# Performance work log

Measured on AMD Instinct MI355X. Metric: run time of the kernel, lower is better.

Reference implementation:

```python
import jax, jax.numpy as jnp
import numpy as np

RES = 7          # pooler_resolution
SR = 2           # sampling_ratio
SCALES = (0.25, 0.125, 0.0625)  # 1/stride for the 3 FPN levels


def _bilinear(feat, ys, xs):
    # feat [C,H,W]; ys, xs [N,S,S] sample coords; returns [C,N,S,S]
    C, H, W = feat.shape
    valid = (ys > -1.0) & (ys < H) & (xs > -1.0) & (xs < W)
    y = jnp.clip(ys, 0.0, H - 1)
    x = jnp.clip(xs, 0.0, W - 1)
    y0 = jnp.floor(y).astype(jnp.int32)
    x0 = jnp.floor(x).astype(jnp.int32)
    y1 = jnp.minimum(y0 + 1, H - 1)
    x1 = jnp.minimum(x0 + 1, W - 1)
    ly = y - y0; lx = x - x0
    hy = 1.0 - ly; hx = 1.0 - lx
    v = (feat[:, y0, x0] * (hy * hx) + feat[:, y0, x1] * (hy * lx)
         + feat[:, y1, x0] * (ly * hx) + feat[:, y1, x1] * (ly * lx))
    return v * valid


def _roi_align(feat, boxes, scale):
    # feat [C,H,W], boxes [N,4] (t,l,b,r) in image coords, aligned=True
    t, l, b, r = (boxes[:, 0], boxes[:, 1], boxes[:, 2], boxes[:, 3])
    sy = t * scale - 0.5
    sx = l * scale - 0.5
    bh = (b - t) * scale / RES
    bw = (r - l) * scale / RES
    S = RES * SR
    g = (jnp.arange(S, dtype=feat.dtype) + 0.5) / SR  # sample offsets in bin units
    ys = sy[:, None] + g[None, :] * bh[:, None]  # [N,S]
    xs = sx[:, None] + g[None, :] * bw[:, None]
    N = boxes.shape[0]
    Y = jnp.broadcast_to(ys[:, :, None], (N, S, S))
    X = jnp.broadcast_to(xs[:, None, :], (N, S, S))
    v = _bilinear(feat, Y, X)                      # [C,N,S,S]
    C = feat.shape[0]
    v = v.reshape(C, N, RES, SR, RES, SR).mean(axis=(3, 5))
    return jnp.transpose(v, (1, 0, 2, 3))          # [N,C,RES,RES]


def _forward(feat0, feat1, feat2, bbox2d, anchor_id,
             fc1_w, fc1_b, bn1_g, bn1_b, fc2_w, fc2_b, bn2_g, bn2_b,
             cate_w, cate_b, bbox3d_w, bbox3d_b, yawc_w, yawc_b,
             yawr_w, yawr_b, hgt_w, hgt_b):
    # yxhw -> tlbr (mu.convert_box_format_yxhw_to_tlbr)
    cy, cx, h, w = (bbox2d[..., 0], bbox2d[..., 1], bbox2d[..., 2], bbox2d[..., 3])
    tlbr = jnp.stack([cy - h / 2, cx - w / 2, cy + h / 2, cx + w / 2], axis=-1)
    level = anchor_id // 3  # [B,N] per-box FPN level (anchor_id // 3 == i routing)
    feats = [feat0, feat1, feat2]
    B, N = level.shape
    C = feat0.shape[1]
    pooled = jnp.zeros((B, N, C, RES, RES), dtype=feat0.dtype)
    for i in range(3):
        al = jax.vmap(lambda fm, bx, s=SCALES[i]: _roi_align(fm, bx, s))(feats[i], tlbr)
        pooled = jnp.where((level == i)[:, :, None, None, None], al, pooled)
    x = pooled.reshape(B * N, -1)  # [B*N, C*RES*RES]
    eps = 1e-5
    for Wt, bb, g2, b2 in ((fc1_w, fc1_b, bn1_g, bn1_b), (fc2_w, fc2_b, bn2_g, bn2_b)):
        x = x @ Wt + bb
        mu = x.mean(0)
        var = x.var(0)
        x = jax.nn.relu((x - mu) / jnp.sqrt(var + eps) * g2 + b2)
    cate = x @ cate_w + cate_b
    bbox3d = x @ bbox3d_w + bbox3d_b
    yawc = x @ yawc_w + yawc_b
    yawr = x @ yawr_w + yawr_b
    hgt = x @ hgt_w + hgt_b
    out = jnp.concatenate([cate, bbox3d, yawc, yawr, hgt], axis=-1)  # [B*N, 100]
    return out.reshape(B, N, -1)


def setup_inputs() -> dict:
    key = jax.random.key(0)
    ks = jax.random.split(key, 24)
    B, N, C = 4, 512, 256
    FC = 1024
    IMG = 512.0
    NUM_CLASSES, BOX_DIM, BINS = 3, 6, 12
    feat0 = jax.random.normal(ks[0], (B, C, 128, 128), jnp.float32)
    feat1 = jax.random.normal(ks[1], (B, C, 64, 64), jnp.float32)
    feat2 = jax.random.normal(ks[2], (B, C, 32, 32), jnp.float32)
    cy = jax.random.uniform(ks[3], (B, N)) * IMG
    cx = jax.random.uniform(ks[4], (B, N)) * IMG
    h = 16.0 + jax.random.uniform(ks[5], (B, N)) * 240.0
    w = 16.0 + jax.random.uniform(ks[6], (B, N)) * 240.0
    bbox2d = jnp.stack([cy, cx, h, w], axis=-1)
    anchor_id = jax.random.randint(ks[7], (B, N), 0, 9, dtype=jnp.int32)
    in_dim = C * RES * RES  # 12544
    fc1_w = jax.random.normal(ks[8], (in_dim, FC), jnp.float32) / np.sqrt(in_dim)
    fc1_b = jnp.zeros((FC,), jnp.float32)
    bn1_g = jnp.ones((FC,), jnp.float32)
    bn1_b = jnp.zeros((FC,), jnp.float32)
    fc2_w = jax.random.normal(ks[9], (FC, FC), jnp.float32) / np.sqrt(FC)
    fc2_b = jnp.zeros((FC,), jnp.float32)
    bn2_g = jnp.ones((FC,), jnp.float32)
    bn2_b = jnp.zeros((FC,), jnp.float32)
    cate_w = jax.random.normal(ks[10], (FC, NUM_CLASSES + 1), jnp.float32) * 0.01
    cate_b = jnp.zeros((NUM_CLASSES + 1,), jnp.float32)
    bbox3d_w = jax.random.normal(ks[11], (FC, NUM_CLASSES * BOX_DIM), jnp.float32) * 0.001
    bbox3d_b = jnp.zeros((NUM_CLASSES * BOX_DIM,), jnp.float32)
    yawc_w = jax.random.normal(ks[12], (FC, NUM_CLASSES * BINS), jnp.float32) * 0.001
    yawc_b = jnp.zeros((NUM_CLASSES * BINS,), jnp.float32)
    yawr_w = jax.random.normal(ks[13], (FC, NUM_CLASSES * BINS), jnp.float32) * 0.001
    yawr_b = jnp.zeros((NUM_CLASSES * BINS,), jnp.float32)
    hgt_w = jax.random.normal(ks[14], (FC, NUM_CLASSES * 2), jnp.float32) * 0.001
    hgt_b = jnp.zeros((NUM_CLASSES * 2,), jnp.float32)
    return {
        'feat0': feat0, 'feat1': feat1, 'feat2': feat2,
        'bbox2d': bbox2d, 'anchor_id': anchor_id,
        'fc1_w': fc1_w, 'fc1_b': fc1_b, 'bn1_g': bn1_g, 'bn1_b': bn1_b,
        'fc2_w': fc2_w, 'fc2_b': fc2_b, 'bn2_g': bn2_g, 'bn2_b': bn2_b,
        'cate_w': cate_w, 'cate_b': cate_b, 'bbox3d_w': bbox3d_w, 'bbox3d_b': bbox3d_b,
        'yawc_w': yawc_w, 'yawc_b': yawc_b, 'yawr_w': yawr_w, 'yawr_b': yawr_b,
        'hgt_w': hgt_w, 'hgt_b': hgt_b,
    }


def reference(feat0, feat1, feat2, bbox2d, anchor_id,
              fc1_w, fc1_b, bn1_g, bn1_b, fc2_w, fc2_b, bn2_g, bn2_b,
              cate_w, cate_b, bbox3d_w, bbox3d_b, yawc_w, yawc_b,
              yawr_w, yawr_b, hgt_w, hgt_b):
    return _forward(feat0, feat1, feat2, bbox2d, anchor_id,
                    fc1_w, fc1_b, bn1_g, bn1_b, fc2_w, fc2_b, bn2_g, bn2_b,
                    cate_w, cate_b, bbox3d_w, bbox3d_b, yawc_w, yawc_b,
                    yawr_w, yawr_b, hgt_w, hgt_b)
```

## Files before the change

kernel.cpp:

```cpp
#include <hip/hip_runtime.h>
#include <hip/hip_bf16.h>

typedef unsigned short u16;
typedef unsigned int u32;
typedef __bf16 bf16x8 __attribute__((ext_vector_type(8)));
typedef float f32x4 __attribute__((ext_vector_type(4)));

#define RESOLUTION 7
#define SR 2
#define SS 14
#define NSAMP 196

static __device__ __forceinline__ u16 f2bf(float f) {
    __hip_bfloat16 t = __float2bfloat16(f);
    return *reinterpret_cast<u16*>(&t);
}
static __device__ __forceinline__ float bf2f(u16 h) {
    return __uint_as_float(((u32)h) << 16);
}

static __device__ __forceinline__ void load_lds16(const u16* g, u16* l) {
    __builtin_amdgcn_global_load_lds(
        (const __attribute__((address_space(1))) unsigned int*)g,
        (__attribute__((address_space(3))) unsigned int*)l, 16, 0, 0);
}

__global__ __launch_bounds__(256) void transpose_feat_kernel(
    const float* __restrict__ in, u16* __restrict__ out, int HW) {
    int b = blockIdx.y;
    int hw0 = blockIdx.x * 64;
    __shared__ u16 tile[256][65];

    int hwo = threadIdx.x & 63;
    int c0 = threadIdx.x >> 6;
    for (int cc = 0; cc < 256; cc += 4) {
        int c = cc + c0;
        float v = in[((size_t)(b * 256 + c)) * HW + hw0 + hwo];
        tile[c][hwo] = f2bf(v);
    }
    __syncthreads();

    int ro = threadIdx.x >> 5;
    int co = (threadIdx.x & 31) * 8;
    for (int i = 0; i < 64; i += 8) {
        int hw = i + ro;
        union { uint4 v; u16 h[8]; } o;
        #pragma unroll
        for (int j = 0; j < 8; ++j) o.h[j] = tile[co + j][hw];
        *(uint4*)&out[((size_t)b * HW + hw0 + hw) * 256 + co] = o.v;
    }
}

__global__ __launch_bounds__(256) void transpose_w_kernel(
    const float* __restrict__ in, u16* __restrict__ out, int K, int perm) {
    int kp0 = blockIdx.x * 64, n0 = blockIdx.y * 64;
    __shared__ u16 tile[64][65];

    int nn = threadIdx.x & 63, ks = threadIdx.x >> 6;
    for (int i = 0; i < 64; i += 4) {
        int kp = kp0 + ks + i;
        int k = perm ? ((kp & 255) * 49 + (kp >> 8)) : kp;
        tile[ks + i][nn] = f2bf(in[(size_t)k * 1024 + n0 + nn]);
    }
    __syncthreads();

    int nw = threadIdx.x >> 3, ko = (threadIdx.x & 7) * 8;
    for (int i = 0; i < 2; ++i) {
        int n = nw + i * 32;
        union { uint4 v; u16 h[8]; } o;
        #pragma unroll
        for (int j = 0; j < 8; ++j) o.h[j] = tile[ko + j][n];
        *(uint4*)&out[(size_t)(n0 + n) * K + kp0 + ko] = o.v;
    }
}

__global__ void head_concat_kernel(
    const float* __restrict__ cate_w, const float* __restrict__ bbox3d_w,
    const float* __restrict__ yawc_w, const float* __restrict__ yawr_w,
    const float* __restrict__ hgt_w,
    const float* __restrict__ cate_b, const float* __restrict__ bbox3d_b,
    const float* __restrict__ yawc_b, const float* __restrict__ yawr_b,
    const float* __restrict__ hgt_b,
    float* __restrict__ wh, float* __restrict__ bh) {
    int idx = blockIdx.x * blockDim.x + threadIdx.x;
    if (idx < 1024 * 100) {
        int k = idx / 100, c = idx % 100;
        float v;
        if (c < 4)        v = cate_w[k * 4 + c];
        else if (c < 22)  v = bbox3d_w[k * 18 + (c - 4)];
        else if (c < 58)  v = yawc_w[k * 36 + (c - 22)];
        else if (c < 94)  v = yawr_w[k * 36 + (c - 58)];
        else              v = hgt_w[k * 6 + (c - 94)];
        wh[idx] = v;
    }
    if (idx < 100) {
        int c = idx;
        float v;
        if (c < 4)        v = cate_b[c];
        else if (c < 22)  v = bbox3d_b[c - 4];
        else if (c < 58)  v = yawc_b[c - 22];
        else if (c < 94)  v = yawr_b[c - 58];
        else              v = hgt_b[c - 94];
        bh[c] = v;
    }
}

__global__ __launch_bounds__(256) void roi_align_v2_kernel(
    const u16* __restrict__ tf0, const u16* __restrict__ tf1,
    const u16* __restrict__ tf2, const float* __restrict__ bbox2d,
    const int* __restrict__ anchor_id, u16* __restrict__ xb) {
    int bn = blockIdx.x;
    int b = bn >> 9;
    int tid = threadIdx.x;

    __shared__ int s_o00[NSAMP], s_o01[NSAMP], s_o10[NSAMP], s_o11[NSAMP];
    __shared__ float s_w00[NSAMP], s_w01[NSAMP], s_w10[NSAMP], s_w11[NSAMP];

    float cy = bbox2d[bn * 4 + 0], cx = bbox2d[bn * 4 + 1];
    float hh = bbox2d[bn * 4 + 2], ww = bbox2d[bn * 4 + 3];
    int lvl = anchor_id[bn] / 3;
    float scale = (lvl == 0) ? 0.25f : ((lvl == 1) ? 0.125f : 0.0625f);
    int H = (lvl == 0) ? 128 : ((lvl == 1) ? 64 : 32);
    int W = H;

    float t = cy - hh * 0.5f, l = cx - ww * 0.5f;
    float btm = cy + hh * 0.5f, r = cx + ww * 0.5f;
    float sy = t * scale - 0.5f, sx = l * scale - 0.5f;
    float bh = (btm - t) * scale * (1.0f / RESOLUTION);
    float bw = (r - l) * scale * (1.0f / RESOLUTION);

    if (tid < NSAMP) {
        int i = tid / SS, j = tid % SS;
        float gi = (i + 0.5f) * (1.0f / SR);
        float gj = (j + 0.5f) * (1.0f / SR);
        float y = sy + gi * bh, x = sx + gj * bw;
        float valid = (y > -1.0f && y < (float)H && x > -1.0f && x < (float)W)
                          ? 0.25f : 0.0f;
        y = fminf(fmaxf(y, 0.0f), (float)(H - 1));
        x = fminf(fmaxf(x, 0.0f), (float)(W - 1));
        int y0 = (int)floorf(y), x0 = (int)floorf(x);
        int y1 = min(y0 + 1, H - 1), x1 = min(x0 + 1, W - 1);
        float ly = y - (float)y0, lx = x - (float)x0;
        float hy = 1.f - ly, hx = 1.f - lx;
        s_o00[tid] = (y0 * W + x0) * 256;
        s_o01[tid] = (y0 * W + x1) * 256;
        s_o10[tid] = (y1 * W + x0) * 256;
        s_o11[tid] = (y1 * W + x1) * 256;
        s_w00[tid] = hy * hx * valid;
        s_w01[tid] = hy * lx * valid;
        s_w10[tid] = ly * hx * valid;
        s_w11[tid] = ly * lx * valid;
    }
    __syncthreads();

    const u16* fb = (lvl == 0) ? (tf0 + (size_t)b * 16384 * 256)
                  : (lvl == 1) ? (tf1 + (size_t)b * 4096 * 256)
                               : (tf2 + (size_t)b * 1024 * 256);
    int g = tid >> 5;
    int c0 = (tid & 31) * 8;
    u16* xr = xb + (size_t)bn * 12544;

    for (int ii = 0; ii < 7; ++ii) {
        int bin = g + ii * 8;
        if (bin >= 49) break;
        int ph = bin / 7, pw = bin % 7;
        float a[8] = {0.f, 0.f, 0.f, 0.f, 0.f, 0.f, 0.f, 0.f};
        #pragma unroll
        for (int dy = 0; dy < SR; ++dy) {
            #pragma unroll
            for (int dx = 0; dx < SR; ++dx) {
                int si = (ph * SR + dy) * SS + (pw * SR + dx);
                int o00 = s_o00[si], o01 = s_o01[si];
                int o10 = s_o10[si], o11 = s_o11[si];
                float w00 = s_w00[si], w01 = s_w01[si];
                float w10 = s_w10[si], w11 = s_w11[si];
                union { uint4 v; u16 h[8]; } u0, u1, u2, u3;
                u0.v = *(const uint4*)(fb + o00 + c0);
                u1.v = *(const uint4*)(fb + o01 + c0);
                u2.v = *(const uint4*)(fb + o10 + c0);
                u3.v = *(const uint4*)(fb + o11 + c0);
                #pragma unroll
                for (int j = 0; j < 8; ++j) {
                    a[j] = fmaf(bf2f(u0.h[j]), w00, a[j]);
                    a[j] = fmaf(bf2f(u1.h[j]), w01, a[j]);
                    a[j] = fmaf(bf2f(u2.h[j]), w10, a[j]);
                    a[j] = fmaf(bf2f(u3.h[j]), w11, a[j]);
                }
            }
        }
        union { uint4 v; u16 h[8]; } o;
        #pragma unroll
        for (int j = 0; j < 8; ++j) o.h[j] = f2bf(a[j]);
        *(uint4*)&xr[bin * 256 + c0] = o.v;
    }
}

__global__ void zero_kernel(float4* __restrict__ p, int n4) {
    int idx = blockIdx.x * blockDim.x + threadIdx.x;
    if (idx < n4) p[idx] = make_float4(0.f, 0.f, 0.f, 0.f);
}

__global__ __launch_bounds__(256) void gemm_splitk_kernel(
    const u16* __restrict__ A, const u16* __restrict__ BT,
    float* __restrict__ Y, int M, int N, int K, int KC) {
    __shared__ u16 la[128 * 32];
    __shared__ u16 lb[128 * 32];
    int m0 = blockIdx.x * 128;
    int n0 = blockIdx.y * 128;
    int kbeg = blockIdx.z * KC;
    int tid = threadIdx.x;
    int w = tid >> 6, lane = tid & 63;
    int wm = (w >> 1) * 64, wn = (w & 1) * 64;

    int idx1 = tid + 256;
    const u16* gA0 = A + (size_t)(m0 + (tid >> 2)) * K + (tid & 3) * 8 + kbeg;
    const u16* gA1 = A + (size_t)(m0 + (idx1 >> 2)) * K + (idx1 & 3) * 8 + kbeg;
    const u16* gB0 = BT + (size_t)(n0 + (tid >> 2)) * K + (tid & 3) * 8 + kbeg;
    const u16* gB1 = BT + (size_t)(n0 + (idx1 >> 2)) * K + (idx1 & 3) * 8 + kbeg;
    u16* lA0 = la + w * 512;
    u16* lA1 = la + 2048 + w * 512;
    u16* lB0 = lb + w * 512;
    u16* lB1 = lb + 2048 + w * 512;

    f32x4 acc[4][4] = {};
    int row16 = lane & 15, q8 = (lane >> 4) * 8;

    for (int k0 = 0; k0 < KC; k0 += 32) {
        load_lds16(gA0 + k0, lA0);
        load_lds16(gA1 + k0, lA1);
        load_lds16(gB0 + k0, lB0);
        load_lds16(gB1 + k0, lB1);
        __syncthreads();

        bf16x8 af[4], bf[4];
        #pragma unroll
        for (int tm = 0; tm < 4; ++tm)
            af[tm] = *(const bf16x8*)&la[(wm + tm * 16 + row16) * 32 + q8];
        #pragma unroll
        for (int tn = 0; tn < 4; ++tn)
            bf[tn] = *(const bf16x8*)&lb[(wn + tn * 16 + row16) * 32 + q8];
        #pragma unroll
        for (int tm = 0; tm < 4; ++tm)
            #pragma unroll
            for (int tn = 0; tn < 4; ++tn)
                acc[tm][tn] = __builtin_amdgcn_mfma_f32_16x16x32_bf16(
                    af[tm], bf[tn], acc[tm][tn], 0, 0, 0);
        __syncthreads();
    }

    int col = lane & 15, qr = lane >> 4;
    #pragma unroll
    for (int tm = 0; tm < 4; ++tm) {
        #pragma unroll
        for (int tn = 0; tn < 4; ++tn) {
            int nn = n0 + wn + tn * 16 + col;
            #pragma unroll
            for (int rg = 0; rg < 4; ++rg) {
                int mm = m0 + wm + tm * 16 + qr * 4 + rg;
                unsafeAtomicAdd(&Y[(size_t)mm * N + nn], acc[tm][tn][rg]);
            }
        }
    }
}

__global__ __launch_bounds__(256) void bn_stats_part_kernel(
    const float* __restrict__ y, float* __restrict__ part, int N) {
    int c4 = blockIdx.x * 256 + (threadIdx.x & 63) * 4;
    int rg = threadIdx.x >> 6;
    int r0 = blockIdx.y * 32;
    float4 s = make_float4(0.f, 0.f, 0.f, 0.f);
    float4 q = make_float4(0.f, 0.f, 0.f, 0.f);
    for (int i = 0; i < 8; ++i) {
        int r = r0 + rg + i * 4;
        float4 v = *(const float4*)&y[(size_t)r * N + c4];
        s.x += v.x; s.y += v.y; s.z += v.z; s.w += v.w;
        q.x += v.x * v.x; q.y += v.y * v.y; q.z += v.z * v.z; q.w += v.w * v.w;
    }
    __shared__ float4 ls[4][64], lq[4][64];
    ls[rg][threadIdx.x & 63] = s;
    lq[rg][threadIdx.x & 63] = q;
    __syncthreads();
    if (rg == 0) {
        int cx = threadIdx.x & 63;
        #pragma unroll
        for (int g = 1; g < 4; ++g) {
            float4 a = ls[g][cx], b = lq[g][cx];
            s.x += a.x; s.y += a.y; s.z += a.z; s.w += a.w;
            q.x += b.x; q.y += b.y; q.z += b.z; q.w += b.w;
        }
        float* po = part + (size_t)blockIdx.y * 2048;
        *(float4*)&po[c4] = s;
        *(float4*)&po[1024 + c4] = q;
    }
}

__global__ __launch_bounds__(256) void bn_stats_final_kernel(
    const float* __restrict__ part, float* __restrict__ stats, int M, int nchunk) {
    int col = blockIdx.x * 256 + threadIdx.x;
    float s = 0.f, q = 0.f;
    for (int ch = 0; ch < nchunk; ++ch) {
        s += part[(size_t)ch * 2048 + col];
        q += part[(size_t)ch * 2048 + 1024 + col];
    }
    float mean = s / (float)M;
    float var = q / (float)M - mean * mean;
    stats[col] = mean;
    stats[1024 + col] = rsqrtf(var + 1e-5f);
}

__global__ void bn_apply_kernel(const float* __restrict__ y,
                                const float* __restrict__ stats,
                                const float* __restrict__ g,
                                const float* __restrict__ b,
                                __hip_bfloat16* __restrict__ xo, int total) {
    int idx = blockIdx.x * blockDim.x + threadIdx.x;
    if (idx >= total) return;
    int col = idx & 1023;
    float v = (y[idx] - stats[col]) * stats[1024 + col] * g[col] + b[col];
    xo[idx] = __float2bfloat16(fmaxf(v, 0.f));
}

__global__ __launch_bounds__(128) void heads_kernel(
    const __hip_bfloat16* __restrict__ x, const float* __restrict__ wh,
    const float* __restrict__ bh, float* __restrict__ out) {
    int m = blockIdx.x;
    __shared__ float lx[1024];
    for (int k = threadIdx.x; k < 1024; k += 128)
        lx[k] = __bfloat162float(x[(size_t)m * 1024 + k]);
    __syncthreads();
    int n = threadIdx.x;
    if (n < 100) {
        float acc = bh[n];
        for (int k = 0; k < 1024; ++k)
            acc += lx[k] * wh[k * 100 + n];
        out[(size_t)m * 100 + n] = acc;
    }
}

extern "C" void kernel_launch(void* const* d_in, const int* in_sizes, int n_in,
                              void* d_out, int out_size, void* d_ws, size_t ws_size,
                              hipStream_t stream) {
    const float* feat0   = (const float*)d_in[0];
    const float* feat1   = (const float*)d_in[1];
    const float* feat2   = (const float*)d_in[2];
    const float* bbox2d  = (const float*)d_in[3];
    const int*   anchor  = (const int*)d_in[4];
    const float* fc1_w   = (const float*)d_in[5];
    const float* bn1_g   = (const float*)d_in[7];
    const float* bn1_b   = (const float*)d_in[8];
    const float* fc2_w   = (const float*)d_in[9];
    const float* bn2_g   = (const float*)d_in[11];
    const float* bn2_b   = (const float*)d_in[12];
    const float* cate_w  = (const float*)d_in[13];
    const float* cate_b  = (const float*)d_in[14];
    const float* bbox3d_w= (const float*)d_in[15];
    const float* bbox3d_b= (const float*)d_in[16];
    const float* yawc_w  = (const float*)d_in[17];
    const float* yawc_b  = (const float*)d_in[18];
    const float* yawr_w  = (const float*)d_in[19];
    const float* yawr_b  = (const float*)d_in[20];
    const float* hgt_w   = (const float*)d_in[21];
    const float* hgt_b   = (const float*)d_in[22];

    const int B = 4, N = 512, FC = 1024;
    const int M = B * N;
    const int K1 = 12544;

    char* base = (char*)d_ws;
    u16* xb = (u16*)base;
    char* ub = base + 51380224;
    u16* tf0 = (u16*)ub;
    u16* tf1 = (u16*)(ub + 33554432);
    u16* tf2 = (u16*)(ub + 41943040);
    u16* w1t = (u16*)ub;
    u16* w2t = (u16*)(ub + 25690112);
    float* y   = (float*)(ub + 27787264);
    u16* x1b = (u16*)(ub + 36175872);
    float* part = (float*)(ub + 40370176);
    char* tail = ub + 44040192;
    float* stats = (float*)tail;
    float* wh    = (float*)(tail + 8192);
    float* bhd   = (float*)(tail + 8192 + 409600);
    float* outp  = (float*)d_out;

    head_concat_kernel<<<(1024 * 100 + 255) / 256, 256, 0, stream>>>(
        cate_w, bbox3d_w, yawc_w, yawr_w, hgt_w,
        cate_b, bbox3d_b, yawc_b, yawr_b, hgt_b, wh, bhd);

    transpose_feat_kernel<<<dim3(16384 / 64, B), 256, 0, stream>>>(feat0, tf0, 16384);
    transpose_feat_kernel<<<dim3(4096 / 64, B),  256, 0, stream>>>(feat1, tf1, 4096);
    transpose_feat_kernel<<<dim3(1024 / 64, B),  256, 0, stream>>>(feat2, tf2, 1024);

    roi_align_v2_kernel<<<M, 256, 0, stream>>>(tf0, tf1, tf2, bbox2d, anchor, xb);

    transpose_w_kernel<<<dim3(K1 / 64, FC / 64), 256, 0, stream>>>(fc1_w, w1t, K1, 1);
    transpose_w_kernel<<<dim3(FC / 64, FC / 64), 256, 0, stream>>>(fc2_w, w2t, FC, 0);

    zero_kernel<<<(M * FC / 4 + 255) / 256, 256, 0, stream>>>((float4*)y, M * FC / 4);
    gemm_splitk_kernel<<<dim3(M / 128, FC / 128, 4), 256, 0, stream>>>(
        xb, w1t, y, M, FC, K1, K1 / 4);
    bn_stats_part_kernel<<<dim3(FC / 256, M / 32), 256, 0, stream>>>(y, part, FC);
    bn_stats_final_kernel<<<FC / 256, 256, 0, stream>>>(part, stats, M, M / 32);
    bn_apply_kernel<<<(M * FC + 255) / 256, 256, 0, stream>>>(
        y, stats, bn1_g, bn1_b, (__hip_bfloat16*)x1b, M * FC);

    zero_kernel<<<(M * FC / 4 + 255) / 256, 256, 0, stream>>>((float4*)y, M * FC / 4);
    gemm_splitk_kernel<<<dim3(M / 128, FC / 128, 4), 256, 0, stream>>>(
        x1b, w2t, y, M, FC, FC, FC / 4);
    bn_stats_part_kernel<<<dim3(FC / 256, M / 32), 256, 0, stream>>>(y, part, FC);
    bn_stats_final_kernel<<<FC / 256, 256, 0, stream>>>(part, stats, M, M / 32);
    bn_apply_kernel<<<(M * FC + 255) / 256, 256, 0, stream>>>(
        y, stats, bn2_g, bn2_b, (__hip_bfloat16*)x1b, M * FC);

    heads_kernel<<<M, 128, 0, stream>>>((const __hip_bfloat16*)x1b, wh, bhd, outp);
}
```

Before: 504.9 us.

## Run prediction heads through split-K MFMA GEMM and raise split-K factor

Replaces the scalar per-row heads kernel with the existing bf16 split-K GEMM. The head weights are packed transposed into bf16, padded to 128 output columns, and an fp32 buffer is pre-seeded with the bias, so the atomically accumulated result is then compacted to 100 columns. It also doubles the split-K factor for both FC GEMMs from 4 to 8 to put more blocks on the GPU. The cost is extra launches, more atomic traffic, and head weights rounded to bf16.

```diff
diff --git a/kernel.cpp b/kernel.cpp
--- a/kernel.cpp
+++ b/kernel.cpp
@@ -81,17 +81,17 @@
     const float* __restrict__ cate_b, const float* __restrict__ bbox3d_b,
     const float* __restrict__ yawc_b, const float* __restrict__ yawr_b,
     const float* __restrict__ hgt_b,
-    float* __restrict__ wh, float* __restrict__ bh) {
+    u16* __restrict__ whT, float* __restrict__ bh) {
     int idx = blockIdx.x * blockDim.x + threadIdx.x;
-    if (idx < 1024 * 100) {
-        int k = idx / 100, c = idx % 100;
-        float v;
-        if (c < 4)        v = cate_w[k * 4 + c];
-        else if (c < 22)  v = bbox3d_w[k * 18 + (c - 4)];
-        else if (c < 58)  v = yawc_w[k * 36 + (c - 22)];
-        else if (c < 94)  v = yawr_w[k * 36 + (c - 58)];
-        else              v = hgt_w[k * 6 + (c - 94)];
-        wh[idx] = v;
+    if (idx < 128 * 1024) {
+        int n = idx >> 10, k = idx & 1023;
+        float v = 0.f;
+        if (n < 4)        v = cate_w[k * 4 + n];
+        else if (n < 22)  v = bbox3d_w[k * 18 + (n - 4)];
+        else if (n < 58)  v = yawc_w[k * 36 + (n - 22)];
+        else if (n < 94)  v = yawr_w[k * 36 + (n - 58)];
+        else if (n < 100) v = hgt_w[k * 6 + (n - 94)];
+        whT[idx] = f2bf(v);
     }
     if (idx < 100) {
         int c = idx;
@@ -200,6 +200,22 @@
     if (idx < n4) p[idx] = make_float4(0.f, 0.f, 0.f, 0.f);
 }
 
+__global__ void bias_init_kernel(float* __restrict__ hout,
+                                 const float* __restrict__ bh, int total) {
+    int idx = blockIdx.x * blockDim.x + threadIdx.x;
+    if (idx >= total) return;
+    int n = idx & 127;
+    hout[idx] = (n < 100) ? bh[n] : 0.f;
+}
+
+__global__ void copy100_kernel(const float* __restrict__ hout,
+                               float* __restrict__ out, int total) {
+    int idx = blockIdx.x * blockDim.x + threadIdx.x;
+    if (idx >= total) return;
+    int m = idx / 100, n = idx - m * 100;
+    out[idx] = hout[m * 128 + n];
+}
+
 __global__ __launch_bounds__(256) void gemm_splitk_kernel(
     const u16* __restrict__ A, const u16* __restrict__ BT,
     float* __restrict__ Y, int M, int N, int K, int KC) {
@@ -318,23 +334,6 @@
     int col = idx & 1023;
     float v = (y[idx] - stats[col]) * stats[1024 + col] * g[col] + b[col];
     xo[idx] = __float2bfloat16(fmaxf(v, 0.f));
-}
-
-__global__ __launch_bounds__(128) void heads_kernel(
-    const __hip_bfloat16* __restrict__ x, const float* __restrict__ wh,
-    const float* __restrict__ bh, float* __restrict__ out) {
-    int m = blockIdx.x;
-    __shared__ float lx[1024];
-    for (int k = threadIdx.x; k < 1024; k += 128)
-        lx[k] = __bfloat162float(x[(size_t)m * 1024 + k]);
-    __syncthreads();
-    int n = threadIdx.x;
-    if (n < 100) {
-        float acc = bh[n];
-        for (int k = 0; k < 1024; ++k)
-            acc += lx[k] * wh[k * 100 + n];
-        out[(size_t)m * 100 + n] = acc;
-    }
 }
 
 extern "C" void kernel_launch(void* const* d_in, const int* in_sizes, int n_in,
@@ -377,15 +376,16 @@
     float* y   = (float*)(ub + 27787264);
     u16* x1b = (u16*)(ub + 36175872);
     float* part = (float*)(ub + 40370176);
+    float* hout = (float*)(ub + 40894464);
     char* tail = ub + 44040192;
     float* stats = (float*)tail;
-    float* wh    = (float*)(tail + 8192);
-    float* bhd   = (float*)(tail + 8192 + 409600);
+    u16*   whT   = (u16*)(tail + 8192);
+    float* bhd   = (float*)(tail + 8192 + 262144);
     float* outp  = (float*)d_out;
 
-    head_concat_kernel<<<(1024 * 100 + 255) / 256, 256, 0, stream>>>(
+    head_concat_kernel<<<(128 * 1024 + 255) / 256, 256, 0, stream>>>(
         cate_w, bbox3d_w, yawc_w, yawr_w, hgt_w,
-        cate_b, bbox3d_b, yawc_b, yawr_b, hgt_b, wh, bhd);
+        cate_b, bbox3d_b, yawc_b, yawr_b, hgt_b, whT, bhd);
 
     transpose_feat_kernel<<<dim3(16384 / 64, B), 256, 0, stream>>>(feat0, tf0, 16384);
     transpose_feat_kernel<<<dim3(4096 / 64, B),  256, 0, stream>>>(feat1, tf1, 4096);
@@ -397,20 +397,23 @@
     transpose_w_kernel<<<dim3(FC / 64, FC / 64), 256, 0, stream>>>(fc2_w, w2t, FC, 0);
 
     zero_kernel<<<(M * FC / 4 + 255) / 256, 256, 0, stream>>>((float4*)y, M * FC / 4);
-    gemm_splitk_kernel<<<dim3(M / 128, FC / 128, 4), 256, 0, stream>>>(
-        xb, w1t, y, M, FC, K1, K1 / 4);
+    gemm_splitk_kernel<<<dim3(M / 128, FC / 128, 8), 256, 0, stream>>>(
+        xb, w1t, y, M, FC, K1, K1 / 8);
     bn_stats_part_kernel<<<dim3(FC / 256, M / 32), 256, 0, stream>>>(y, part, FC);
     bn_stats_final_kernel<<<FC / 256, 256, 0, stream>>>(part, stats, M, M / 32);
     bn_apply_kernel<<<(M * FC + 255) / 256, 256, 0, stream>>>(
         y, stats, bn1_g, bn1_b, (__hip_bfloat16*)x1b, M * FC);
 
     zero_kernel<<<(M * FC / 4 + 255) / 256, 256, 0, stream>>>((float4*)y, M * FC / 4);
-    gemm_splitk_kernel<<<dim3(M / 128, FC / 128, 4), 256, 0, stream>>>(
-        x1b, w2t, y, M, FC, FC, FC / 4);
+    gemm_splitk_kernel<<<dim3(M / 128, FC / 128, 8), 256, 0, stream>>>(
+        x1b, w2t, y, M, FC, FC, FC / 8);
     bn_stats_part_kernel<<<dim3(FC / 256, M / 32), 256, 0, stream>>>(y, part, FC);
     bn_stats_final_kernel<<<FC / 256, 256, 0, stream>>>(part, stats, M, M / 32);
     bn_apply_kernel<<<(M * FC + 255) / 256, 256, 0, stream>>>(
         y, stats, bn2_g, bn2_b, (__hip_bfloat16*)x1b, M * FC);
 
-    heads_kernel<<<M, 128, 0, stream>>>((const __hip_bfloat16*)x1b, wh, bhd, outp);
-}
+    bias_init_kernel<<<(M * 128 + 255) / 256, 256, 0, stream>>>(hout, bhd, M * 128);
+    gemm_splitk_kernel<<<dim3(M / 128, 1, 8), 256, 0, stream>>>(
+        x1b, whT, hout, M, 128, FC, FC / 8);
+    copy100_kernel<<<(M * 100 + 255) / 256, 256, 0, stream>>>(hout, outp, M * 100);
+}
```

Result: slower. 524.7 us (+3.9%).
